# Optimization experiments

Hardware: AMD Instinct MI355X
Metric: run time of the kernel (lower is better)

Reference implementation:

```python
import jax, jax.numpy as jnp
import numpy as np

HEAD_SIZE = 64
D_MODEL = 768


def setup_inputs() -> dict:
    key = jax.random.key(0)
    ks = jax.random.split(key, 7)
    x = jax.random.normal(ks[0], (8, 4096, D_MODEL), dtype=jnp.float32)
    def lin_init(kw, kb, fan_in, fan_out):
        bound = 1.0 / np.sqrt(fan_in)
        W = jax.random.uniform(kw, (fan_in, fan_out), minval=-bound, maxval=bound, dtype=jnp.float32)
        b = jax.random.uniform(kb, (fan_out,), minval=-bound, maxval=bound, dtype=jnp.float32)
        return W, b
    Wq, bq = lin_init(ks[1], ks[2], D_MODEL, HEAD_SIZE)
    Wk, bk = lin_init(ks[3], ks[4], D_MODEL, HEAD_SIZE)
    Wv, bv = lin_init(ks[5], ks[6], D_MODEL, HEAD_SIZE)
    return {"x": x, "Wq": Wq, "bq": bq, "Wk": Wk, "bk": bk, "Wv": Wv, "bv": bv}


def reference(x, Wq, bq, Wk, bk, Wv, bv):
    # x: [B, N, 768]; projections to [B, N, head_size]
    q = jnp.einsum("bnd,dh->bnh", x, Wq) + bq
    k = jnp.einsum("bnd,dh->bnh", x, Wk) + bk
    v = jnp.einsum("bnd,dh->bnh", x, Wv) + bv
    scale = 1.0 / jnp.sqrt(jnp.asarray(q.shape[-1], dtype=q.dtype))
    wei = jnp.einsum("bqh,bkh->bqk", q, k) * scale  # [B, N, N]
    wei = jax.nn.softmax(wei, axis=-1)
    out = jnp.einsum("bqk,bkh->bqh", wei, v)  # [B, N, head_size]
    return out
```

## Files before the change

kernel.cpp:

```cpp
#include <hip/hip_runtime.h>
#include <stdint.h>
#include <stddef.h>

typedef __bf16 bf16x8 __attribute__((ext_vector_type(8)));
typedef __bf16 bf16x4 __attribute__((ext_vector_type(4)));
typedef float  f32x4  __attribute__((ext_vector_type(4)));

#define MFMA16(A, B, C) __builtin_amdgcn_mfma_f32_16x16x32_bf16((A), (B), (C), 0, 0, 0)

#define QSCALE 0.18033688011112042f

#if __has_builtin(__builtin_amdgcn_exp2f)
__device__ __forceinline__ float fast_exp2(float x) {
    return __builtin_amdgcn_exp2f(x);
}
#else
__device__ __forceinline__ float fast_exp2(float x) {
    float r;
    asm("v_exp_f32 %0, %1" : "=v"(r) : "v"(x));
    return r;
}
#endif

__global__ __launch_bounds__(256) void qkv_proj_kernel(
    const float* __restrict__ x,
    const float* __restrict__ Wq, const float* __restrict__ bq,
    const float* __restrict__ Wk, const float* __restrict__ bk,
    const float* __restrict__ Wv, const float* __restrict__ bv,
    __bf16* __restrict__ Qg, __bf16* __restrict__ Kg, __bf16* __restrict__ Vpg)
{
    __shared__ __bf16 xs[64][40];
    __shared__ __bf16 wt[192][40];

    const int tid  = threadIdx.x;
    const int wid  = tid >> 6;
    const int lane = tid & 63;
    const int l15  = lane & 15;
    const int l4   = lane >> 4;
    const int m0   = blockIdx.x * 64;

    f32x4 acc[4][3];
    #pragma unroll
    for (int i = 0; i < 4; ++i)
        #pragma unroll
        for (int j = 0; j < 3; ++j)
            acc[i][j] = (f32x4){0.f, 0.f, 0.f, 0.f};

    for (int k0 = 0; k0 < 768; k0 += 32) {
        #pragma unroll
        for (int i = 0; i < 2; ++i) {
            int idx = tid + 256 * i;
            int row = idx >> 3;
            int c4  = idx & 7;
            const float4 v = *reinterpret_cast<const float4*>(
                x + (size_t)(m0 + row) * 768 + k0 + c4 * 4);
            bf16x4 t;
            t[0] = (__bf16)v.x; t[1] = (__bf16)v.y;
            t[2] = (__bf16)v.z; t[3] = (__bf16)v.w;
            *reinterpret_cast<bf16x4*>(&xs[row][c4 * 4]) = t;
        }
        #pragma unroll
        for (int i = 0; i < 6; ++i) {
            int idx = tid + 256 * i;
            int kg  = idx / 192;
            int c   = idx - kg * 192;
            const float* Wm = (c < 64) ? Wq : ((c < 128) ? Wk : Wv);
            int cc = c & 63;
            bf16x4 t;
            #pragma unroll
            for (int j = 0; j < 4; ++j)
                t[j] = (__bf16)Wm[(size_t)(k0 + kg * 4 + j) * 64 + cc];
            *reinterpret_cast<bf16x4*>(&wt[c][kg * 4]) = t;
        }
        __syncthreads();

        bf16x8 afrag[4];
        #pragma unroll
        for (int rf = 0; rf < 4; ++rf)
            afrag[rf] = *reinterpret_cast<const bf16x8*>(&xs[rf * 16 + l15][l4 * 8]);
        #pragma unroll
        for (int cf = 0; cf < 3; ++cf) {
            bf16x8 bfrag = *reinterpret_cast<const bf16x8*>(
                &wt[wid * 48 + cf * 16 + l15][l4 * 8]);
            #pragma unroll
            for (int rf = 0; rf < 4; ++rf)
                acc[rf][cf] = MFMA16(afrag[rf], bfrag, acc[rf][cf]);
        }
        __syncthreads();
    }

    #pragma unroll
    for (int cf = 0; cf < 3; ++cf) {
        int col = wid * 48 + cf * 16 + l15;
        int mi  = col >> 6;
        int h   = col & 63;
        float bias = (mi == 0) ? bq[h] : ((mi == 1) ? bk[h] : bv[h]);
        float scl  = (mi == 0) ? QSCALE : 1.0f;
        #pragma unroll
        for (int rf = 0; rf < 4; ++rf) {
            int r0 = rf * 16 + l4 * 4;
            if (mi == 2) {
                int m  = m0 + r0;
                int bb = m >> 12;
                int n0 = m & 4095;
                int n0p = (n0 & ~31) | (l4 * 8 + (rf & 1) * 4);
                bf16x4 t;
                #pragma unroll
                for (int r = 0; r < 4; ++r)
                    t[r] = (__bf16)(acc[rf][cf][r] + bias);
                *reinterpret_cast<bf16x4*>(
                    Vpg + ((size_t)bb * 64 + h) * 4096 + n0p) = t;
            } else {
                __bf16* G = (mi == 0) ? Qg : Kg;
                #pragma unroll
                for (int r = 0; r < 4; ++r)
                    G[(size_t)(m0 + r0 + r) * 64 + h] =
                        (__bf16)((acc[rf][cf][r] + bias) * scl);
            }
        }
    }
}

__global__ __launch_bounds__(512, 4) void attn_kernel(
    const __bf16* __restrict__ Qg, const __bf16* __restrict__ Kg,
    const __bf16* __restrict__ Vpg, float* __restrict__ out)
{
    __shared__ __align__(16) char smem[65536];
    __bf16* ksbase = reinterpret_cast<__bf16*>(smem);
    __bf16* vsbase = ksbase + 4 * 2 * 32 * 64;

    const int tid  = threadIdx.x;
    const int wid  = tid >> 6;
    const int lane = tid & 63;
    const int l15  = lane & 15;
    const int l4   = lane >> 4;
    const int qw2  = wid & 1;
    const int ks   = wid >> 1;
    const int b    = blockIdx.x & 7;
    const int qb   = blockIdx.x >> 3;
    const int q0   = qb * 64 + qw2 * 32;

    const __bf16* Kb = Kg  + (size_t)b * 4096 * 64;
    const __bf16* Vb = Vpg + (size_t)b * 64 * 4096;

    __bf16* kst0 = ksbase + (ks * 2 + 0) * 32 * 64;
    __bf16* kst1 = ksbase + (ks * 2 + 1) * 32 * 64;
    __bf16* vst0 = vsbase + (ks * 2 + 0) * 64 * 32;
    __bf16* vst1 = vsbase + (ks * 2 + 1) * 64 * 32;

    int koff[2][2], voff[4];
    #pragma unroll
    for (int dc = 0; dc < 2; ++dc)
        #pragma unroll
        for (int cf = 0; cf < 2; ++cf) {
            int row = cf * 16 + l15;
            koff[dc][cf] = row * 64 + (((dc * 4 + l4) ^ (row & 7)) * 8);
        }
    #pragma unroll
    for (int ht = 0; ht < 4; ++ht) {
        int row = ht * 16 + l15;
        voff[ht] = row * 32 + ((l4 ^ (row & 3)) * 8);
    }

    bf16x8 aq[2][2];
    #pragma unroll
    for (int set = 0; set < 2; ++set)
        #pragma unroll
        for (int dc = 0; dc < 2; ++dc)
            aq[set][dc] = *reinterpret_cast<const bf16x8*>(
                Qg + (size_t)(b * 4096 + q0 + set * 16 + l15) * 64 + dc * 32 + l4 * 8);

    f32x4 lacc0 = (f32x4){0.f, 0.f, 0.f, 0.f};
    f32x4 lacc1 = (f32x4){0.f, 0.f, 0.f, 0.f};
    f32x4 o[2][4];
    #pragma unroll
    for (int set = 0; set < 2; ++set)
        #pragma unroll
        for (int ht = 0; ht < 4; ++ht)
            o[set][ht] = (f32x4){0.f, 0.f, 0.f, 0.f};

    bf16x8 kreg[2], vreg[2];
    const int kl_row = lane >> 3;
    const int kl_g   = lane & 7;
    const int vl_row = lane >> 2;
    const int vl_g   = lane & 3;

    auto stage_load = [&](int c) {
        #pragma unroll
        for (int i2 = 0; i2 < 2; ++i2) {
            int i = qw2 * 2 + i2;
            kreg[i2] = *reinterpret_cast<const bf16x8*>(
                Kb + (size_t)(c * 32 + i * 8 + kl_row) * 64 + kl_g * 8);
            vreg[i2] = *reinterpret_cast<const bf16x8*>(
                Vb + (size_t)(i * 16 + vl_row) * 4096 + c * 32 + vl_g * 8);
        }
    };
    auto stage_write = [&](__bf16* kp, __bf16* vp) {
        #pragma unroll
        for (int i2 = 0; i2 < 2; ++i2) {
            int i  = qw2 * 2 + i2;
            int kr = i * 8 + kl_row;
            int vr = i * 16 + vl_row;
            *reinterpret_cast<bf16x8*>(kp + kr * 64 + ((kl_g ^ kl_row) * 8)) = kreg[i2];
            *reinterpret_cast<bf16x8*>(vp + vr * 32 + ((vl_g ^ (vl_row & 3)) * 8)) = vreg[i2];
        }
    };

    const int c0 = ks * 32;
    stage_load(c0);
    stage_write(kst0, vst0);

    for (int t = 0; t < 32; ++t) {
        __syncthreads();
        const __bf16* kp = (t & 1) ? kst1 : kst0;
        const __bf16* vp = (t & 1) ? vst1 : vst0;
        __bf16* kpn = (t & 1) ? kst0 : kst1;
        __bf16* vpn = (t & 1) ? vst0 : vst1;
        const bool pre = (t + 1) < 32;
        if (pre) stage_load(c0 + t + 1);

        f32x4 s0[2], s1[2];
        #pragma unroll
        for (int cf = 0; cf < 2; ++cf) {
            s0[cf] = (f32x4){0.f, 0.f, 0.f, 0.f};
            s1[cf] = (f32x4){0.f, 0.f, 0.f, 0.f};
        }
        __builtin_amdgcn_s_setprio(1);
        #pragma unroll
        for (int dc = 0; dc < 2; ++dc)
            #pragma unroll
            for (int cf = 0; cf < 2; ++cf) {
                bf16x8 kf = *reinterpret_cast<const bf16x8*>(kp + koff[dc][cf]);
                s0[cf] = MFMA16(kf, aq[0][dc], s0[cf]);
                s1[cf] = MFMA16(kf, aq[1][dc], s1[cf]);
            }
        __builtin_amdgcn_s_setprio(0);

        #pragma unroll
        for (int cf = 0; cf < 2; ++cf)
            #pragma unroll
            for (int r = 0; r < 4; ++r) {
                s0[cf][r] = fast_exp2(s0[cf][r]);
                s1[cf][r] = fast_exp2(s1[cf][r]);
            }
        lacc0 += s0[0]; lacc0 += s0[1];
        lacc1 += s1[0]; lacc1 += s1[1];

        bf16x8 pb0, pb1;
        #pragma unroll
        for (int j = 0; j < 4; ++j) {
            pb0[j]     = (__bf16)s0[0][j];
            pb0[j + 4] = (__bf16)s0[1][j];
            pb1[j]     = (__bf16)s1[0][j];
            pb1[j + 4] = (__bf16)s1[1][j];
        }

        __builtin_amdgcn_s_setprio(1);
        #pragma unroll
        for (int ht = 0; ht < 4; ++ht) {
            bf16x8 vf = *reinterpret_cast<const bf16x8*>(vp + voff[ht]);
            o[0][ht] = MFMA16(vf, pb0, o[0][ht]);
            o[1][ht] = MFMA16(vf, pb1, o[1][ht]);
        }
        __builtin_amdgcn_s_setprio(0);

        if (pre) stage_write(kpn, vpn);
    }

    float l0 = lacc0[0] + lacc0[1] + lacc0[2] + lacc0[3];
    float l1 = lacc1[0] + lacc1[1] + lacc1[2] + lacc1[3];
    l0 += __shfl_xor(l0, 16); l0 += __shfl_xor(l0, 32);
    l1 += __shfl_xor(l1, 16); l1 += __shfl_xor(l1, 32);

    __syncthreads();
    float* lbuf = reinterpret_cast<float*>(smem);
    float* smO  = lbuf + 256;

    if (l4 == 0) {
        lbuf[((qw2 * 2 + 0) * 4 + ks) * 16 + l15] = l0;
        lbuf[((qw2 * 2 + 1) * 4 + ks) * 16 + l15] = l1;
    }
    const int hcol = 4 * l4;
    if (ks != 0) {
        #pragma unroll
        for (int set = 0; set < 2; ++set)
            #pragma unroll
            for (int ht = 0; ht < 4; ++ht)
                *reinterpret_cast<f32x4*>(
                    &smO[(((ks - 1) * 2 + qw2) * 32 + set * 16 + l15) * 68
                         + ht * 16 + hcol]) = o[set][ht];
    }
    __syncthreads();
    if (ks == 0) {
        #pragma unroll
        for (int set = 0; set < 2; ++set) {
            float L = lbuf[((qw2 * 2 + set) * 4 + 0) * 16 + l15]
                    + lbuf[((qw2 * 2 + set) * 4 + 1) * 16 + l15]
                    + lbuf[((qw2 * 2 + set) * 4 + 2) * 16 + l15]
                    + lbuf[((qw2 * 2 + set) * 4 + 3) * 16 + l15];
            float inv = 1.0f / L;
            #pragma unroll
            for (int ht = 0; ht < 4; ++ht) {
                f32x4 acc = o[set][ht];
                #pragma unroll
                for (int k = 1; k < 4; ++k) {
                    f32x4 p = *reinterpret_cast<const f32x4*>(
                        &smO[(((k - 1) * 2 + qw2) * 32 + set * 16 + l15) * 68
                             + ht * 16 + hcol]);
                    acc[0] += p[0]; acc[1] += p[1]; acc[2] += p[2]; acc[3] += p[3];
                }
                acc[0] *= inv; acc[1] *= inv; acc[2] *= inv; acc[3] *= inv;
                *reinterpret_cast<f32x4*>(
                    out + (size_t)(b * 4096 + q0 + set * 16 + l15) * 64
                        + ht * 16 + hcol) = acc;
            }
        }
    }
}

extern "C" void kernel_launch(void* const* d_in, const int* in_sizes, int n_in,
                              void* d_out, int out_size, void* d_ws, size_t ws_size,
                              hipStream_t stream)
{
    (void)in_sizes; (void)n_in; (void)out_size; (void)ws_size;
    const float* x  = (const float*)d_in[0];
    const float* Wq = (const float*)d_in[1];
    const float* bq = (const float*)d_in[2];
    const float* Wk = (const float*)d_in[3];
    const float* bk = (const float*)d_in[4];
    const float* Wv = (const float*)d_in[5];
    const float* bv = (const float*)d_in[6];
    float* out = (float*)d_out;

    __bf16* Qg  = (__bf16*)d_ws;
    __bf16* Kg  = Qg + (size_t)32768 * 64;
    __bf16* Vpg = Kg + (size_t)32768 * 64;

    qkv_proj_kernel<<<512, 256, 0, stream>>>(x, Wq, bq, Wk, bk, Wv, bv, Qg, Kg, Vpg);
    attn_kernel<<<512, 512, 0, stream>>>(Qg, Kg, Vpg, out);
}
```

Baseline: 78.61 us.

## Load K/V fragments directly from global into registers, drop LDS staging

Replaces the double-buffered shared-memory staging of K and V tiles, along with its per-iteration barriers, with per-wave direct global loads of the MFMA fragments into registers, prefetched one step ahead. LDS use shrinks to what the final reduction needs, which can allow more resident blocks, and the per-step syncthreads go away. The cost is that the two waves sharing a key split now each load the same K/V data, doubling global/L2 traffic, and the fragment loads are less coalesced (16-byte reads strided by rows, with V strided by 4096 elements). The prefetch on the last iteration wraps around and loads data that is never used.

```diff
diff --git a/kernel.cpp b/kernel.cpp
--- a/kernel.cpp
+++ b/kernel.cpp
@@ -125,9 +125,7 @@
     const __bf16* __restrict__ Qg, const __bf16* __restrict__ Kg,
     const __bf16* __restrict__ Vpg, float* __restrict__ out)
 {
-    __shared__ __align__(16) char smem[65536];
-    __bf16* ksbase = reinterpret_cast<__bf16*>(smem);
-    __bf16* vsbase = ksbase + 4 * 2 * 32 * 64;
+    __shared__ __align__(16) float smem[13312];
 
     const int tid  = threadIdx.x;
     const int wid  = tid >> 6;
@@ -143,25 +141,6 @@
     const __bf16* Kb = Kg  + (size_t)b * 4096 * 64;
     const __bf16* Vb = Vpg + (size_t)b * 64 * 4096;
 
-    __bf16* kst0 = ksbase + (ks * 2 + 0) * 32 * 64;
-    __bf16* kst1 = ksbase + (ks * 2 + 1) * 32 * 64;
-    __bf16* vst0 = vsbase + (ks * 2 + 0) * 64 * 32;
-    __bf16* vst1 = vsbase + (ks * 2 + 1) * 64 * 32;
-
-    int koff[2][2], voff[4];
-    #pragma unroll
-    for (int dc = 0; dc < 2; ++dc)
-        #pragma unroll
-        for (int cf = 0; cf < 2; ++cf) {
-            int row = cf * 16 + l15;
-            koff[dc][cf] = row * 64 + (((dc * 4 + l4) ^ (row & 7)) * 8);
-        }
-    #pragma unroll
-    for (int ht = 0; ht < 4; ++ht) {
-        int row = ht * 16 + l15;
-        voff[ht] = row * 32 + ((l4 ^ (row & 3)) * 8);
-    }
-
     bf16x8 aq[2][2];
     #pragma unroll
     for (int set = 0; set < 2; ++set)
@@ -179,45 +158,28 @@
         for (int ht = 0; ht < 4; ++ht)
             o[set][ht] = (f32x4){0.f, 0.f, 0.f, 0.f};
 
-    bf16x8 kreg[2], vreg[2];
-    const int kl_row = lane >> 3;
-    const int kl_g   = lane & 7;
-    const int vl_row = lane >> 2;
-    const int vl_g   = lane & 3;
-
-    auto stage_load = [&](int c) {
-        #pragma unroll
-        for (int i2 = 0; i2 < 2; ++i2) {
-            int i = qw2 * 2 + i2;
-            kreg[i2] = *reinterpret_cast<const bf16x8*>(
-                Kb + (size_t)(c * 32 + i * 8 + kl_row) * 64 + kl_g * 8);
-            vreg[i2] = *reinterpret_cast<const bf16x8*>(
-                Vb + (size_t)(i * 16 + vl_row) * 4096 + c * 32 + vl_g * 8);
-        }
+    bf16x8 kf[2][2], vf[4];
+    auto kload = [&](int c) {
+        #pragma unroll
+        for (int dc = 0; dc < 2; ++dc)
+            #pragma unroll
+            for (int cf = 0; cf < 2; ++cf)
+                kf[dc][cf] = *reinterpret_cast<const bf16x8*>(
+                    Kb + (size_t)(c * 32 + cf * 16 + l15) * 64 + dc * 32 + l4 * 8);
     };
-    auto stage_write = [&](__bf16* kp, __bf16* vp) {
-        #pragma unroll
-        for (int i2 = 0; i2 < 2; ++i2) {
-            int i  = qw2 * 2 + i2;
-            int kr = i * 8 + kl_row;
-            int vr = i * 16 + vl_row;
-            *reinterpret_cast<bf16x8*>(kp + kr * 64 + ((kl_g ^ kl_row) * 8)) = kreg[i2];
-            *reinterpret_cast<bf16x8*>(vp + vr * 32 + ((vl_g ^ (vl_row & 3)) * 8)) = vreg[i2];
-        }
+    auto vload = [&](int c) {
+        #pragma unroll
+        for (int ht = 0; ht < 4; ++ht)
+            vf[ht] = *reinterpret_cast<const bf16x8*>(
+                Vb + (size_t)(ht * 16 + l15) * 4096 + c * 32 + l4 * 8);
     };
 
     const int c0 = ks * 32;
-    stage_load(c0);
-    stage_write(kst0, vst0);
+    kload(c0);
+    vload(c0);
 
     for (int t = 0; t < 32; ++t) {
-        __syncthreads();
-        const __bf16* kp = (t & 1) ? kst1 : kst0;
-        const __bf16* vp = (t & 1) ? vst1 : vst0;
-        __bf16* kpn = (t & 1) ? kst0 : kst1;
-        __bf16* vpn = (t & 1) ? vst0 : vst1;
-        const bool pre = (t + 1) < 32;
-        if (pre) stage_load(c0 + t + 1);
+        const int cn = c0 + ((t + 1) & 31);
 
         f32x4 s0[2], s1[2];
         #pragma unroll
@@ -230,11 +192,12 @@
         for (int dc = 0; dc < 2; ++dc)
             #pragma unroll
             for (int cf = 0; cf < 2; ++cf) {
-                bf16x8 kf = *reinterpret_cast<const bf16x8*>(kp + koff[dc][cf]);
-                s0[cf] = MFMA16(kf, aq[0][dc], s0[cf]);
-                s1[cf] = MFMA16(kf, aq[1][dc], s1[cf]);
+                s0[cf] = MFMA16(kf[dc][cf], aq[0][dc], s0[cf]);
+                s1[cf] = MFMA16(kf[dc][cf], aq[1][dc], s1[cf]);
             }
         __builtin_amdgcn_s_setprio(0);
+
+        kload(cn);
 
         #pragma unroll
         for (int cf = 0; cf < 2; ++cf)
@@ -258,13 +221,12 @@
         __builtin_amdgcn_s_setprio(1);
         #pragma unroll
         for (int ht = 0; ht < 4; ++ht) {
-            bf16x8 vf = *reinterpret_cast<const bf16x8*>(vp + voff[ht]);
-            o[0][ht] = MFMA16(vf, pb0, o[0][ht]);
-            o[1][ht] = MFMA16(vf, pb1, o[1][ht]);
+            o[0][ht] = MFMA16(vf[ht], pb0, o[0][ht]);
+            o[1][ht] = MFMA16(vf[ht], pb1, o[1][ht]);
         }
         __builtin_amdgcn_s_setprio(0);
 
-        if (pre) stage_write(kpn, vpn);
+        vload(cn);
     }
 
     float l0 = lacc0[0] + lacc0[1] + lacc0[2] + lacc0[3];
@@ -272,9 +234,8 @@
     l0 += __shfl_xor(l0, 16); l0 += __shfl_xor(l0, 32);
     l1 += __shfl_xor(l1, 16); l1 += __shfl_xor(l1, 32);
 
-    __syncthreads();
-    float* lbuf = reinterpret_cast<float*>(smem);
-    float* smO  = lbuf + 256;
+    float* lbuf = smem;
+    float* smO  = smem + 256;
 
     if (l4 == 0) {
         lbuf[((qw2 * 2 + 0) * 4 + ks) * 16 + l15] = l0;
```

Result: slower. 152.4 us (+93.9%).
